# Kernel tuning notes

Hardware: AMD Instinct MI355X
Metric: run time of the kernel (lower is better)

Reference implementation:

```python
import jax, jax.numpy as jnp
import numpy as np

H = 200  # hidden size


def _init(k, shape):
    bound = 1.0 / np.sqrt(H)
    return jax.random.uniform(k, shape, jnp.float32, -bound, bound)


def setup_inputs() -> dict:
    key = jax.random.key(0)
    ks = jax.random.split(key, 11)
    T, B, D = 784, 512, 1
    x = jax.random.normal(ks[0], (T, 1, B, D), jnp.float32)
    return {
        "x": x,
        "W_in": _init(ks[1], (H, D)),
        "b_in": _init(ks[2], (H,)),
        # PyTorch LSTM gate order: i, f, g, o. b = b_ih + b_hh folded together.
        "Wih_f": _init(ks[3], (4 * H, H)),
        "Whh_f": _init(ks[4], (4 * H, H)),
        "b_f": _init(ks[5], (4 * H,)),
        "Wih_b": _init(ks[6], (4 * H, H)),
        "Whh_b": _init(ks[7], (4 * H, H)),
        "b_b": _init(ks[8], (4 * H,)),
        "W_fc": _init(ks[9], (10, 2 * H)),
        "b_fc": _init(ks[10], (10,)),
    }


def _lstm_dir(gates_in, Whh, reverse):
    # gates_in: (T, B, 4H) = x @ Wih.T + b, precomputed outside the scan.
    B = gates_in.shape[1]
    h0 = jnp.zeros((B, H), gates_in.dtype)

    def step(carry, g_in):
        h, c = carry
        g = g_in + h @ Whh.T  # (B, 4H)
        i, f, gg, o = jnp.split(g, 4, axis=-1)
        c = jax.nn.sigmoid(f) * c + jax.nn.sigmoid(i) * jnp.tanh(gg)
        h = jax.nn.sigmoid(o) * jnp.tanh(c)
        return (h, c), h

    _, hs = jax.lax.scan(step, (h0, h0), gates_in, reverse=reverse)
    return hs  # (T, B, H)


def reference(x, W_in, b_in, Wih_f, Whh_f, b_f, Wih_b, Whh_b, b_b, W_fc, b_fc):
    x = jnp.squeeze(x, 1)            # (T, B, D)
    x = x @ W_in.T + b_in            # (T, B, H)  input projection
    gf = x @ Wih_f.T + b_f           # (T, B, 4H) precomputed input gates, fwd dir
    gb = x @ Wih_b.T + b_b           # (T, B, 4H) precomputed input gates, bwd dir
    hf = _lstm_dir(gf, Whh_f, reverse=False)
    hb = _lstm_dir(gb, Whh_b, reverse=True)
    h = jnp.concatenate([hf, hb], axis=-1)  # (T, B, 2H)
    out = h @ W_fc.T + b_fc                 # (T, B, 10)
    return out.mean(axis=1)                 # (T, 10) -- matches x.mean(1)
```

## Files before the change

### kernel.cpp

```cpp
#include <hip/hip_runtime.h>


typedef short short8 __attribute__((ext_vector_type(8)));
typedef float f32x4 __attribute__((ext_vector_type(4)));
typedef unsigned short ushort_t;

#define T_STEPS 784
#define BATCH   512
#define HID     200
#define NKT     7
#define NMT     50
#define THREADS 512
#define HBUF    3584
#define NLDST   18
#define DYN_LDS (2 * HBUF * 2 + NLDST * NKT * 512 * 2)

#define WS_HSUM 0
#define WS_UV   1254400
#define WS_WSW  (1254400 + 12800)

__device__ __forceinline__ ushort_t f2bf(float f) {
  union { float f; unsigned u; } x; x.f = f;
  return (ushort_t)((x.u + 0x7FFFu + ((x.u >> 16) & 1u)) >> 16);
}
__device__ __forceinline__ float bf2f(ushort_t u) {
  union { unsigned u; float f; } x; x.u = (unsigned)u << 16; return x.f;
}

__device__ __forceinline__ float row16_sum(float v) {
  union { float f; int i; } a, b;
  a.f = v;
  b.i = __builtin_amdgcn_update_dpp(0, a.i, 0x118, 0xF, 0xF, true); a.f += b.f;
  b.i = __builtin_amdgcn_update_dpp(0, a.i, 0x114, 0xF, 0xF, true); a.f += b.f;
  b.i = __builtin_amdgcn_update_dpp(0, a.i, 0x112, 0xF, 0xF, true); a.f += b.f;
  b.i = __builtin_amdgcn_update_dpp(0, a.i, 0x111, 0xF, 0xF, true); a.f += b.f;
  return a.f;
}

__global__ void prep_uv(const float* __restrict__ Wih_f, const float* __restrict__ b_f,
                        const float* __restrict__ Wih_b, const float* __restrict__ b_b,
                        const float* __restrict__ W_in, const float* __restrict__ b_in,
                        float* __restrict__ uv_g) {
  const int dir = blockIdx.x, j = threadIdx.x;
  if (j >= HID) return;
  const float* Wih = dir ? Wih_b : Wih_f;
  const float* b   = dir ? b_b   : b_f;
  for (int q = 0; q < 4; ++q) {
    const int row = q * HID + j;
    const float* wr = Wih + (size_t)row * HID;
    float u = 0.f, v = 0.f;
    for (int k = 0; k < HID; ++k) {
      u = fmaf(wr[k], W_in[k], u);
      v = fmaf(wr[k], b_in[k], v);
    }
    uv_g[(size_t)dir * 1600 + j * 8 + q]     = u;
    uv_g[(size_t)dir * 1600 + j * 8 + 4 + q] = v + b[row];
  }
}

__global__ void prep_w(const float* __restrict__ Whh_f, const float* __restrict__ Whh_b,
                       const float* __restrict__ uv_g, ushort_t* __restrict__ w_sw) {
  const int bid = blockIdx.x, lane = threadIdx.x;
  const int dir = bid / (NMT * NKT);
  const int rem = bid % (NMT * NKT);
  const int mt = rem / NKT, kt = rem % NKT;
  const float* W = dir ? Whh_b : Whh_f;
  const int m = lane & 15;
  const int q = m & 3;
  const int j = mt * 4 + (m >> 2);
  const int row = q * HID + j;
  const int grp = lane >> 4;
  short8 v8 = {0, 0, 0, 0, 0, 0, 0, 0};
  if (kt < 6) {
#pragma unroll
    for (int e = 0; e < 8; ++e)
      v8[e] = (short)f2bf(W[(size_t)row * HID + kt * 32 + grp * 8 + e]);
  } else if (grp == 0) {
#pragma unroll
    for (int e = 0; e < 8; ++e)
      v8[e] = (short)f2bf(W[(size_t)row * HID + 192 + e]);
  } else if (grp == 1) {
    const float U = uv_g[(size_t)dir * 1600 + j * 8 + q];
    const float V = uv_g[(size_t)dir * 1600 + j * 8 + 4 + q];
    const ushort_t vhi = f2bf(V), uhi = f2bf(U);
    v8[0] = (short)vhi;
    v8[1] = (short)f2bf(V - bf2f(vhi));
    v8[2] = (short)uhi;
    v8[3] = (short)f2bf(U - bf2f(uhi));
    v8[4] = (short)uhi;
  }
  *(short8*)(w_sw + (size_t)bid * 512 + (size_t)lane * 8) = v8;
}

__device__ __forceinline__ void cell_update(const f32x4 a, const int haddr,
                                            ushort_t* __restrict__ hnext,
                                            float& c, float& hold) {
  const float L1 = 1.44269504088896340736f;
  const float ei = __builtin_amdgcn_exp2f(fminf(-L1 * a[0], 30.f));
  const float ef = __builtin_amdgcn_exp2f(fminf(-L1 * a[1], 30.f));
  const float eg = __builtin_amdgcn_exp2f(fminf(-2.f * L1 * a[2], 30.f));
  const float eo = __builtin_amdgcn_exp2f(fminf(-L1 * a[3], 30.f));
  const float pi = 1.f + ei, pf = 1.f + ef, pg = 1.f + eg;
  const float pig = pi * pg;
  const float R1 = __builtin_amdgcn_rcpf(pig * pf);
  const float sf = pig * R1;
  const float sitg = (1.f - eg) * pf * R1;
  const float cn = fmaf(sf, c, sitg);
  c = cn;
  const float ec = __builtin_amdgcn_exp2f(fminf(-2.f * L1 * cn, 83.f));
  const float R2 = __builtin_amdgcn_rcpf((1.f + ec) * (1.f + eo));
  const float h = (1.f - ec) * R2;
  hnext[haddr] = f2bf(h);
  hold = row16_sum(h);
}

template <int NLDS>
__device__ __forceinline__ void scan_loop(
    const int rbase, const int lfirst, const int dir, const int b0,
    const int lane, const int wv, const ushort_t* __restrict__ wg,
    const float* __restrict__ x, float* __restrict__ hsum,
    ushort_t* __restrict__ h_lds, const ushort_t* __restrict__ w_lds_my) {
  constexpr int NREG = 4;
  constexpr int NT = NREG + NLDS;
  const int bcol = lane & 15, krow = lane >> 4;
  const bool xw = (wv == 0) & (krow == 1);

  short8 wreg[NREG][NKT];
#pragma unroll
  for (int it = 0; it < NREG; ++it)
#pragma unroll
    for (int kt = 0; kt < NKT; ++kt)
      wreg[it][kt] =
          *(const short8*)(wg + ((size_t)((rbase + it) * NKT + kt)) * 512 + lane * 8);
#pragma unroll
  for (int it = 0; it < NREG; ++it)
#pragma unroll
    for (int kt = 0; kt < NKT; ++kt)
      asm volatile("" : "+v"(wreg[it][kt]));

  int haddr[NT];
#pragma unroll
  for (int i = 0; i < NT; ++i) {
    const int tile = (i < NREG) ? rbase + i : lfirst + (i - NREG);
    const int j = tile * 4 + krow;
    haddr[i] = (j >> 5) * 512 + (bcol | (((j >> 3) & 3) << 4)) * 8 + (j & 7);
  }

  float c[NT], hold[NT];
#pragma unroll
  for (int i = 0; i < NT; ++i) { c[i] = 0.f; hold[i] = 0.f; }

  const int dcol = dir * HID;
  const int jb = rbase * 4 + krow;
  const int jl = lfirst * 4 + krow;
  int t_prev = 0, cur = 0;

  for (int s = 0; s < T_STEPS; ++s) {
    const int t = dir ? (T_STEPS - 1 - s) : s;

    if (s > 0 && bcol == 15) {
#pragma unroll
      for (int i = 0; i < NREG; ++i)
        atomicAdd(&hsum[(size_t)t_prev * 400 + dcol + jb + 4 * i], hold[i]);
#pragma unroll
      for (int i = 0; i < NLDS; ++i)
        atomicAdd(&hsum[(size_t)t_prev * 400 + dcol + jl + 4 * i], hold[NREG + i]);
    }

    const int sn = (s + 1 < T_STEPS) ? s + 1 : s;
    float xn = 0.f;
    if (xw) xn = x[(size_t)(dir ? T_STEPS - 1 - sn : sn) * BATCH + b0 + bcol];

    short8 bf[NKT];
#pragma unroll
    for (int kt = 0; kt < NKT; ++kt)
      bf[kt] = *(const short8*)&h_lds[cur * HBUF + kt * 512 + lane * 8];

    ushort_t* hnext = h_lds + (cur ^ 1) * HBUF;

    if (xw) {
      const ushort_t hi = f2bf(xn);
      const ushort_t lo = f2bf(xn - bf2f(hi));
      const int sb = 6 * 512 + lane * 8;
      hnext[sb + 2] = hi;
      hnext[sb + 3] = hi;
      hnext[sb + 4] = lo;
    }

#pragma unroll
    for (int p = 0; p + 1 < NREG; p += 2) {
      f32x4 a0 = {0.f, 0.f, 0.f, 0.f}, a1 = {0.f, 0.f, 0.f, 0.f};
#pragma unroll
      for (int kt = 0; kt < NKT; ++kt) {
        a0 = __builtin_amdgcn_mfma_f32_16x16x32_bf16(wreg[p][kt],     bf[kt], a0, 0, 0, 0);
        a1 = __builtin_amdgcn_mfma_f32_16x16x32_bf16(wreg[p + 1][kt], bf[kt], a1, 0, 0, 0);
      }
      cell_update(a0, haddr[p],     hnext, c[p],     hold[p]);
      cell_update(a1, haddr[p + 1], hnext, c[p + 1], hold[p + 1]);
    }
#pragma unroll
    for (int p = 0; p + 1 < NLDS; p += 2) {
      const int i0 = NREG + p, i1 = NREG + p + 1;
      f32x4 a0 = {0.f, 0.f, 0.f, 0.f}, a1 = {0.f, 0.f, 0.f, 0.f};
#pragma unroll
      for (int kt = 0; kt < NKT; ++kt) {
        const short8 af0 = *(const short8*)&w_lds_my[((p)     * NKT + kt) * 512 + lane * 8];
        const short8 af1 = *(const short8*)&w_lds_my[((p + 1) * NKT + kt) * 512 + lane * 8];
        a0 = __builtin_amdgcn_mfma_f32_16x16x32_bf16(af0, bf[kt], a0, 0, 0, 0);
        a1 = __builtin_amdgcn_mfma_f32_16x16x32_bf16(af1, bf[kt], a1, 0, 0, 0);
      }
      cell_update(a0, haddr[i0], hnext, c[i0], hold[i0]);
      cell_update(a1, haddr[i1], hnext, c[i1], hold[i1]);
    }
    if constexpr (NLDS & 1) {
      constexpr int p = NLDS - 1;
      const int i0 = NREG + p;
      f32x4 a0 = {0.f, 0.f, 0.f, 0.f};
#pragma unroll
      for (int kt = 0; kt < NKT; ++kt) {
        const short8 af = *(const short8*)&w_lds_my[(p * NKT + kt) * 512 + lane * 8];
        a0 = __builtin_amdgcn_mfma_f32_16x16x32_bf16(af, bf[kt], a0, 0, 0, 0);
      }
      cell_update(a0, haddr[i0], hnext, c[i0], hold[i0]);
    }

    t_prev = t;
    __syncthreads();
    cur ^= 1;
  }
  if (bcol == 15) {
#pragma unroll
    for (int i = 0; i < NREG; ++i)
      atomicAdd(&hsum[(size_t)t_prev * 400 + dcol + jb + 4 * i], hold[i]);
#pragma unroll
    for (int i = 0; i < NLDS; ++i)
      atomicAdd(&hsum[(size_t)t_prev * 400 + dcol + jl + 4 * i], hold[NREG + i]);
  }
}

__global__ __launch_bounds__(THREADS) void lstm_main(
    const float* __restrict__ x, const ushort_t* __restrict__ w_sw,
    float* __restrict__ hsum) {
  extern __shared__ __align__(16) ushort_t dynlds[];
  ushort_t* h_lds = dynlds;
  ushort_t* w_lds = dynlds + 2 * HBUF;

  const int tid = threadIdx.x;
  const int lane = tid & 63;
  const int wv = tid >> 6;
  const int dir = blockIdx.x & 1;
  const int b0 = (blockIdx.x >> 1) * 16;

  const ushort_t* wg = w_sw + (size_t)dir * NMT * NKT * 512;

  for (int i = tid; i < HBUF; i += THREADS) ((unsigned*)h_lds)[i] = 0;
  for (int i = tid; i < NLDST * NKT * 64; i += THREADS)
    *(short8*)&w_lds[(size_t)i * 8] =
        *(const short8*)(wg + (size_t)32 * NKT * 512 + (size_t)i * 8);
  __syncthreads();

  if (tid < 16) {
    const int t0 = dir ? T_STEPS - 1 : 0;
    const float x0 = x[(size_t)t0 * BATCH + b0 + tid];
    const ushort_t hi = f2bf(x0);
    const ushort_t lo = f2bf(x0 - bf2f(hi));
    const int sb = 6 * 512 + (16 + tid) * 8;
    h_lds[sb + 0] = 0x3F80; h_lds[sb + 1] = 0x3F80;
    h_lds[HBUF + sb + 0] = 0x3F80; h_lds[HBUF + sb + 1] = 0x3F80;
    h_lds[sb + 2] = hi; h_lds[sb + 3] = hi; h_lds[sb + 4] = lo;
  }
  __syncthreads();

  const int rbase = 4 * wv;
  const int lfirst = (wv < 6) ? (32 + 2 * wv) : (44 + 3 * (wv - 6));
  const ushort_t* wl = w_lds + (size_t)(lfirst - 32) * NKT * 512;
  if (wv < 6)
    scan_loop<2>(rbase, lfirst, dir, b0, lane, wv, wg, x, hsum, h_lds, wl);
  else
    scan_loop<3>(rbase, lfirst, dir, b0, lane, wv, wg, x, hsum, h_lds, wl);
}

__global__ void out_proj(const float* __restrict__ hsum, const float* __restrict__ Wfc,
                         const float* __restrict__ bfc, float* __restrict__ out) {
  const int t = blockIdx.x, tid = threadIdx.x;
  float a[10] = {0.f, 0.f, 0.f, 0.f, 0.f, 0.f, 0.f, 0.f, 0.f, 0.f};
  for (int col = tid; col < 400; col += 256) {
    const float hv = hsum[(size_t)t * 400 + col] * (1.f / 512.f);
#pragma unroll
    for (int o = 0; o < 10; ++o) a[o] = fmaf(hv, Wfc[o * 400 + col], a[o]);
  }
#pragma unroll
  for (int o = 0; o < 10; ++o) {
    float v = a[o];
    for (int m = 32; m; m >>= 1) v += __shfl_xor(v, m);
    a[o] = v;
  }
  __shared__ float red[4][10];
  if ((tid & 63) == 0)
#pragma unroll
    for (int o = 0; o < 10; ++o) red[tid >> 6][o] = a[o];
  __syncthreads();
  if (tid < 10)
    out[t * 10 + tid] = bfc[tid] + red[0][tid] + red[1][tid] + red[2][tid] + red[3][tid];
}

extern "C" void kernel_launch(void* const* d_in, const int* in_sizes, int n_in,
                              void* d_out, int out_size, void* d_ws, size_t ws_size,
                              hipStream_t stream) {
  const float* x     = (const float*)d_in[0];
  const float* W_in  = (const float*)d_in[1];
  const float* b_in  = (const float*)d_in[2];
  const float* Wih_f = (const float*)d_in[3];
  const float* Whh_f = (const float*)d_in[4];
  const float* b_f   = (const float*)d_in[5];
  const float* Wih_b = (const float*)d_in[6];
  const float* Whh_b = (const float*)d_in[7];
  const float* b_b   = (const float*)d_in[8];
  const float* W_fc  = (const float*)d_in[9];
  const float* b_fc  = (const float*)d_in[10];
  float* out = (float*)d_out;

  char* ws = (char*)d_ws;
  float*    hsum = (float*)(ws + WS_HSUM);
  float*    uv_g = (float*)(ws + WS_UV);
  ushort_t* w_sw = (ushort_t*)(ws + WS_WSW);

  hipFuncSetAttribute((const void*)lstm_main,
                      hipFuncAttributeMaxDynamicSharedMemorySize, DYN_LDS);

  hipMemsetAsync(hsum, 0, (size_t)T_STEPS * 400 * sizeof(float), stream);
  prep_uv<<<2, 256, 0, stream>>>(Wih_f, b_f, Wih_b, b_b, W_in, b_in, uv_g);
  prep_w<<<2 * NMT * NKT, 64, 0, stream>>>(Whh_f, Whh_b, uv_g, w_sw);
  lstm_main<<<64, THREADS, DYN_LDS, stream>>>(x, w_sw, hsum);
  out_proj<<<T_STEPS, 256, 0, stream>>>(hsum, W_fc, b_fc, out);
}
```

Baseline: 1.675 ms.

## Pin register-resident weight tiles in AGPRs via inline-asm MFMA

Loads the register-cached recurrent weight fragments straight into fixed accumulation registers (a0-a111) and issues the MFMAs through inline assembly that reads the A operand from those AGPRs. The LDS-weight MFMAs also become inline asm, with manual s_nop hazard padding. Launch bounds now request 2 waves per SIMD, which frees VGPR pressure and could allow more co-resident blocks. In exchange, the manual nops add latency each step, the compiler can no longer schedule these instructions, and hazard handling is now the programmer's responsibility.

```diff
diff --git a/kernel.cpp b/kernel.cpp
--- a/kernel.cpp
+++ b/kernel.cpp
@@ -36,6 +36,46 @@
   b.i = __builtin_amdgcn_update_dpp(0, a.i, 0x111, 0xF, 0xF, true); a.f += b.f;
   return a.f;
 }
+
+#define PIN1(T, K, N0, N1, N2, N3)                                            \
+  {                                                                           \
+    union { short8 s; unsigned u[4]; } cv;                                    \
+    cv.s = *(const short8*)(wg +                                              \
+        ((size_t)((rbase + (T)) * NKT + (K))) * 512 + lane * 8);              \
+    asm volatile("v_accvgpr_write_b32 a" #N0 ", %0\n\t"                       \
+                 "v_accvgpr_write_b32 a" #N1 ", %1\n\t"                       \
+                 "v_accvgpr_write_b32 a" #N2 ", %2\n\t"                       \
+                 "v_accvgpr_write_b32 a" #N3 ", %3"                           \
+                 :: "v"(cv.u[0]), "v"(cv.u[1]), "v"(cv.u[2]), "v"(cv.u[3])    \
+                 : "a" #N0, "a" #N1, "a" #N2, "a" #N3);                       \
+  }
+
+#define MF(N0, N1, N2, N3, ACC, B)                                            \
+  asm volatile("v_mfma_f32_16x16x32_bf16 %0, a[" #N0 ":" #N3 "], %1, %0"      \
+               : "+v"(ACC) : "v"(B)                                           \
+               : "a" #N0, "a" #N1, "a" #N2, "a" #N3)
+#define MFS(N0, N1, N2, N3, ACC, B)                                           \
+  asm volatile("s_nop 1\n\t"                                                  \
+               "v_mfma_f32_16x16x32_bf16 %0, a[" #N0 ":" #N3 "], %1, %0"      \
+               : "+v"(ACC) : "v"(B)                                           \
+               : "a" #N0, "a" #N1, "a" #N2, "a" #N3)
+#define MFE(N0, N1, N2, N3, ACC, B)                                           \
+  asm volatile("v_mfma_f32_16x16x32_bf16 %0, a[" #N0 ":" #N3 "], %1, %0\n\t"  \
+               "s_nop 7\n\ts_nop 7"                                           \
+               : "+v"(ACC) : "v"(B)                                           \
+               : "a" #N0, "a" #N1, "a" #N2, "a" #N3)
+
+#define MFV(ACC, A, B)                                                        \
+  asm volatile("v_mfma_f32_16x16x32_bf16 %0, %1, %2, %0"                      \
+               : "+v"(ACC) : "v"(A), "v"(B))
+#define MFVS(ACC, A, B)                                                       \
+  asm volatile("s_nop 1\n\t"                                                  \
+               "v_mfma_f32_16x16x32_bf16 %0, %1, %2, %0"                      \
+               : "+v"(ACC) : "v"(A), "v"(B))
+#define MFVE(ACC, A, B)                                                       \
+  asm volatile("v_mfma_f32_16x16x32_bf16 %0, %1, %2, %0\n\t"                  \
+               "s_nop 7\n\ts_nop 7"                                           \
+               : "+v"(ACC) : "v"(A), "v"(B))
 
 __global__ void prep_uv(const float* __restrict__ Wih_f, const float* __restrict__ b_f,
                         const float* __restrict__ Wih_b, const float* __restrict__ b_b,
@@ -125,18 +165,23 @@
   const int bcol = lane & 15, krow = lane >> 4;
   const bool xw = (wv == 0) & (krow == 1);
 
-  short8 wreg[NREG][NKT];
-#pragma unroll
-  for (int it = 0; it < NREG; ++it)
-#pragma unroll
-    for (int kt = 0; kt < NKT; ++kt)
-      wreg[it][kt] =
-          *(const short8*)(wg + ((size_t)((rbase + it) * NKT + kt)) * 512 + lane * 8);
-#pragma unroll
-  for (int it = 0; it < NREG; ++it)
-#pragma unroll
-    for (int kt = 0; kt < NKT; ++kt)
-      asm volatile("" : "+v"(wreg[it][kt]));
+  PIN1(0, 0,  0,  1,  2,  3)  PIN1(0, 1,  4,  5,  6,  7)
+  PIN1(0, 2,  8,  9, 10, 11)  PIN1(0, 3, 12, 13, 14, 15)
+  PIN1(0, 4, 16, 17, 18, 19)  PIN1(0, 5, 20, 21, 22, 23)
+  PIN1(0, 6, 24, 25, 26, 27)
+  PIN1(1, 0, 28, 29, 30, 31)  PIN1(1, 1, 32, 33, 34, 35)
+  PIN1(1, 2, 36, 37, 38, 39)  PIN1(1, 3, 40, 41, 42, 43)
+  PIN1(1, 4, 44, 45, 46, 47)  PIN1(1, 5, 48, 49, 50, 51)
+  PIN1(1, 6, 52, 53, 54, 55)
+  PIN1(2, 0, 56, 57, 58, 59)  PIN1(2, 1, 60, 61, 62, 63)
+  PIN1(2, 2, 64, 65, 66, 67)  PIN1(2, 3, 68, 69, 70, 71)
+  PIN1(2, 4, 72, 73, 74, 75)  PIN1(2, 5, 76, 77, 78, 79)
+  PIN1(2, 6, 80, 81, 82, 83)
+  PIN1(3, 0, 84, 85, 86, 87)  PIN1(3, 1, 88, 89, 90, 91)
+  PIN1(3, 2, 92, 93, 94, 95)  PIN1(3, 3, 96, 97, 98, 99)
+  PIN1(3, 4, 100, 101, 102, 103)  PIN1(3, 5, 104, 105, 106, 107)
+  PIN1(3, 6, 108, 109, 110, 111)
+  asm volatile("s_nop 7\n\ts_nop 7");
 
   int haddr[NT];
 #pragma unroll
@@ -145,7 +190,6 @@
     const int j = tile * 4 + krow;
     haddr[i] = (j >> 5) * 512 + (bcol | (((j >> 3) & 3) << 4)) * 8 + (j & 7);
   }
-
   float c[NT], hold[NT];
 #pragma unroll
   for (int i = 0; i < NT; ++i) { c[i] = 0.f; hold[i] = 0.f; }
@@ -187,27 +231,49 @@
       hnext[sb + 4] = lo;
     }
 
-#pragma unroll
-    for (int p = 0; p + 1 < NREG; p += 2) {
+    {
       f32x4 a0 = {0.f, 0.f, 0.f, 0.f}, a1 = {0.f, 0.f, 0.f, 0.f};
-#pragma unroll
-      for (int kt = 0; kt < NKT; ++kt) {
-        a0 = __builtin_amdgcn_mfma_f32_16x16x32_bf16(wreg[p][kt],     bf[kt], a0, 0, 0, 0);
-        a1 = __builtin_amdgcn_mfma_f32_16x16x32_bf16(wreg[p + 1][kt], bf[kt], a1, 0, 0, 0);
-      }
-      cell_update(a0, haddr[p],     hnext, c[p],     hold[p]);
-      cell_update(a1, haddr[p + 1], hnext, c[p + 1], hold[p + 1]);
+      MFS(0, 1, 2, 3, a0, bf[0]);      MFS(28, 29, 30, 31, a1, bf[0]);
+      MF(4, 5, 6, 7, a0, bf[1]);       MF(32, 33, 34, 35, a1, bf[1]);
+      MF(8, 9, 10, 11, a0, bf[2]);     MF(36, 37, 38, 39, a1, bf[2]);
+      MF(12, 13, 14, 15, a0, bf[3]);   MF(40, 41, 42, 43, a1, bf[3]);
+      MF(16, 17, 18, 19, a0, bf[4]);   MF(44, 45, 46, 47, a1, bf[4]);
+      MF(20, 21, 22, 23, a0, bf[5]);   MF(48, 49, 50, 51, a1, bf[5]);
+      MFE(24, 25, 26, 27, a0, bf[6]);  MFE(52, 53, 54, 55, a1, bf[6]);
+      cell_update(a0, haddr[0], hnext, c[0], hold[0]);
+      cell_update(a1, haddr[1], hnext, c[1], hold[1]);
+    }
+    {
+      f32x4 a0 = {0.f, 0.f, 0.f, 0.f}, a1 = {0.f, 0.f, 0.f, 0.f};
+      MFS(56, 57, 58, 59, a0, bf[0]);  MFS(84, 85, 86, 87, a1, bf[0]);
+      MF(60, 61, 62, 63, a0, bf[1]);   MF(88, 89, 90, 91, a1, bf[1]);
+      MF(64, 65, 66, 67, a0, bf[2]);   MF(92, 93, 94, 95, a1, bf[2]);
+      MF(68, 69, 70, 71, a0, bf[3]);   MF(96, 97, 98, 99, a1, bf[3]);
+      MF(72, 73, 74, 75, a0, bf[4]);   MF(100, 101, 102, 103, a1, bf[4]);
+      MF(76, 77, 78, 79, a0, bf[5]);   MF(104, 105, 106, 107, a1, bf[5]);
+      MFE(80, 81, 82, 83, a0, bf[6]);  MFE(108, 109, 110, 111, a1, bf[6]);
+      cell_update(a0, haddr[2], hnext, c[2], hold[2]);
+      cell_update(a1, haddr[3], hnext, c[3], hold[3]);
     }
 #pragma unroll
     for (int p = 0; p + 1 < NLDS; p += 2) {
       const int i0 = NREG + p, i1 = NREG + p + 1;
       f32x4 a0 = {0.f, 0.f, 0.f, 0.f}, a1 = {0.f, 0.f, 0.f, 0.f};
-#pragma unroll
-      for (int kt = 0; kt < NKT; ++kt) {
+      {
+        const short8 af0 = *(const short8*)&w_lds_my[((p)     * NKT + 0) * 512 + lane * 8];
+        const short8 af1 = *(const short8*)&w_lds_my[((p + 1) * NKT + 0) * 512 + lane * 8];
+        MFVS(a0, af0, bf[0]);  MFVS(a1, af1, bf[0]);
+      }
+#pragma unroll
+      for (int kt = 1; kt < NKT - 1; ++kt) {
         const short8 af0 = *(const short8*)&w_lds_my[((p)     * NKT + kt) * 512 + lane * 8];
         const short8 af1 = *(const short8*)&w_lds_my[((p + 1) * NKT + kt) * 512 + lane * 8];
-        a0 = __builtin_amdgcn_mfma_f32_16x16x32_bf16(af0, bf[kt], a0, 0, 0, 0);
-        a1 = __builtin_amdgcn_mfma_f32_16x16x32_bf16(af1, bf[kt], a1, 0, 0, 0);
+        MFV(a0, af0, bf[kt]);  MFV(a1, af1, bf[kt]);
+      }
+      {
+        const short8 af0 = *(const short8*)&w_lds_my[((p)     * NKT + 6) * 512 + lane * 8];
+        const short8 af1 = *(const short8*)&w_lds_my[((p + 1) * NKT + 6) * 512 + lane * 8];
+        MFVE(a0, af0, bf[6]);  MFVE(a1, af1, bf[6]);
       }
       cell_update(a0, haddr[i0], hnext, c[i0], hold[i0]);
       cell_update(a1, haddr[i1], hnext, c[i1], hold[i1]);
@@ -216,10 +282,18 @@
       constexpr int p = NLDS - 1;
       const int i0 = NREG + p;
       f32x4 a0 = {0.f, 0.f, 0.f, 0.f};
-#pragma unroll
-      for (int kt = 0; kt < NKT; ++kt) {
+      {
+        const short8 af = *(const short8*)&w_lds_my[(p * NKT + 0) * 512 + lane * 8];
+        MFVS(a0, af, bf[0]);
+      }
+#pragma unroll
+      for (int kt = 1; kt < NKT - 1; ++kt) {
         const short8 af = *(const short8*)&w_lds_my[(p * NKT + kt) * 512 + lane * 8];
-        a0 = __builtin_amdgcn_mfma_f32_16x16x32_bf16(af, bf[kt], a0, 0, 0, 0);
+        MFV(a0, af, bf[kt]);
+      }
+      {
+        const short8 af = *(const short8*)&w_lds_my[(p * NKT + 6) * 512 + lane * 8];
+        MFVE(a0, af, bf[6]);
       }
       cell_update(a0, haddr[i0], hnext, c[i0], hold[i0]);
     }
@@ -238,7 +312,7 @@
   }
 }
 
-__global__ __launch_bounds__(THREADS) void lstm_main(
+__global__ __launch_bounds__(THREADS, 2) void lstm_main(
     const float* __restrict__ x, const ushort_t* __restrict__ w_sw,
     float* __restrict__ hsum) {
   extern __shared__ __align__(16) ushort_t dynlds[];
```

Measured after the change: 1.835 ms. +9.5%, slower.
